# Performance work log

Measured on AMD Instinct MI355X. Metric: run time of the kernel, lower is better.

## Reference

```python
import jax, jax.numpy as jnp
import numpy as np

B, N, H, E, C = 32, 128, 8, 64, 16
D = H * E  # d_model


def auto_head_configs(n_heads, patch_num):
    candidates = set()
    for d in range(1, patch_num + 1):
        for K in (3, 5, 7):
            eff = (K - 1) * d + 1
            if eff <= patch_num and K <= patch_num and (K % 2 == 1):
                candidates.add((K, d, eff))
    gk = patch_num if patch_num % 2 == 1 else patch_num - 1
    gk = max(1, gk)
    candidates.add((gk, 1, gk))
    candidates = sorted(candidates, key=lambda x: (x[2], -x[0], x[1]))
    if not candidates:
        return [(1, 1)] * n_heads
    configs = []
    for h in range(n_heads):
        idx = round(h * (len(candidates) - 1) / max(1, n_heads - 1))
        idx = min(idx, len(candidates) - 1)
        configs.append((candidates[idx][0], candidates[idx][1]))
    return configs


def build_na_mask(n_heads, patch_num):
    mask = np.zeros((n_heads, patch_num, patch_num), dtype=bool)
    for h, (K, d) in enumerate(auto_head_configs(n_heads, patch_num)):
        pos = np.arange(patch_num)[:, None]                      # [N,1]
        ideal = pos + (np.arange(K) - K // 2) * d                # [N,K]
        valid = (ideal >= 0) & (ideal < patch_num)
        rows = np.broadcast_to(pos, ideal.shape)
        mask[h, rows[valid], ideal[valid]] = True
    return mask


def setup_inputs() -> dict:
    key = jax.random.key(0)
    kq, kk, kv, k1, k2 = jax.random.split(key, 5)
    return {
        "queries": jax.random.normal(kq, (B, N, H, E), dtype=jnp.float32),
        "keys": jax.random.normal(kk, (B, C, N, H, E), dtype=jnp.float32),
        "values": jax.random.normal(kv, (B, C, N, H, E), dtype=jnp.float32),
        "w1": jax.random.normal(k1, (D, D // 4), dtype=jnp.float32) * 0.02,
        "b1": jnp.zeros((D // 4,), dtype=jnp.float32),
        "w2": jax.random.normal(k2, (D // 4, 1), dtype=jnp.float32) * 0.02,
        "b2": jnp.zeros((1,), dtype=jnp.float32),
        "na_mask": jnp.asarray(build_na_mask(H, N)),  # [H,N,N] bool
    }


def reference(queries, keys, values, w1, b1, w2, b2, na_mask):
    Bb, Nn, Hh, Ee = queries.shape
    Cc = keys.shape[1]
    scale = Ee ** (-0.5)
    # per-exo-variable gate from mean-pooled values
    v_pool = values.mean(axis=2).reshape(Bb, Cc, Hh * Ee)           # [B,C,D]
    hid = jax.nn.gelu(v_pool @ w1 + b1, approximate=False)
    gate = jax.nn.sigmoid(hid @ w2 + b2)                             # [B,C,1]
    q = queries.transpose(0, 2, 1, 3)                                # [B,H,N,E]
    k_cat = keys.transpose(0, 3, 1, 2, 4).reshape(Bb, Hh, Cc * Nn, Ee)
    v_g = values * gate[:, :, :, None, None]                         # [B,C,N,H,E]
    v_cat = v_g.transpose(0, 3, 1, 2, 4).reshape(Bb, Hh, Cc * Nn, Ee)
    # mask [H,N,N] -> [H,N,C*N] (same neighborhood replicated per exo var)
    tmask = jnp.broadcast_to(na_mask[:, :, None, :], (Hh, Nn, Cc, Nn)).reshape(Hh, Nn, Cc * Nn)
    attn = jnp.einsum('bhne,bhme->bhnm', q, k_cat) * scale
    attn = jnp.where(tmask, attn, -jnp.inf)
    attn = jax.nn.softmax(attn, axis=-1)
    out = jnp.einsum('bhnm,bhme->bhne', attn, v_cat)
    return out.transpose(0, 2, 1, 3)                                 # [B,N,H,E]
```

## Files before the change

### kernel.cpp

```cpp
#include <hip/hip_runtime.h>
#include <hip/hip_bf16.h>
#include <math.h>

#define BB 32
#define NN 128
#define HH 8
#define EE 64
#define CC 16
#define DD 512

#define NEG_BIG (-1.0e30f)

__device__ __forceinline__ float bf2f(unsigned short u) {
    union { unsigned int i; float f; } x; x.i = ((unsigned int)u) << 16; return x.f;
}
__device__ __forceinline__ float bflo(unsigned int u) {
    union { unsigned int i; float f; } x; x.i = u << 16; return x.f;
}
__device__ __forceinline__ float bfhi(unsigned int u) {
    union { unsigned int i; float f; } x; x.i = u & 0xffff0000u; return x.f;
}
__device__ __forceinline__ unsigned short f2bf(float f) {
    union { float f; unsigned int i; } x; x.f = f;
    unsigned int r = x.i + 0x7fffu + ((x.i >> 16) & 1u);
    return (unsigned short)(r >> 16);
}

template <bool F32>
__device__ __forceinline__ float ldx(const void* p, int i) {
    if constexpr (F32) return ((const float*)p)[i];
    else               return bf2f(((const unsigned short*)p)[i]);
}

__device__ __forceinline__ void wave_lds_sync() {
    asm volatile("s_waitcnt lgkmcnt(0)" ::: "memory");
    __builtin_amdgcn_wave_barrier();
}

__device__ const int g_dil[8] = {1, 5, 19, 14, 37, 23, 55, 63};

__global__ void detect_dtype(const unsigned short* __restrict__ q, int* __restrict__ flag) {
    const int lane = threadIdx.x;
    int outliers = 0;
    #pragma unroll
    for (int i = 0; i < 16; ++i) {
        unsigned short u = q[(i * 64 + lane) * 2];
        int e = (u >> 7) & 0xFF;
        int sane = (e >= 101 && e <= 140) || ((u & 0x7FFFu) == 0);
        outliers += !sane;
    }
    #pragma unroll
    for (int m = 32; m >= 1; m >>= 1) outliers += __shfl_xor(outliers, m, 64);
    if (lane == 0) *flag = (outliers > 256) ? 1 : 0;
}

template <bool F32>
__global__ __launch_bounds__(1024) void gate_kernel(
    const void* __restrict__ values,
    const void* __restrict__ w1,
    const void* __restrict__ b1,
    const void* __restrict__ w2,
    const void* __restrict__ b2,
    const int*  __restrict__ flag,
    float* __restrict__ gate_out)
{
    if (*flag != (F32 ? 1 : 0)) return;
    __shared__ float vps[4][DD];
    __shared__ float vp[DD];
    __shared__ float hidp[4][DD / 4];
    __shared__ float hid[DD / 4];
    const int bc  = blockIdx.x;
    const int t   = threadIdx.x;
    const int grp = t >> 8;
    const int tt  = t & 255;
    float a0 = 0.f, a1 = 0.f;
    if constexpr (F32) {
        const float2* vb = (const float2*)((const float*)values + (size_t)bc * NN * DD)
                           + (size_t)(grp * 32) * (DD / 2);
        #pragma unroll 8
        for (int n = 0; n < 32; ++n) { float2 u = vb[n * (DD / 2) + tt]; a0 += u.x; a1 += u.y; }
    } else {
        const unsigned int* vb = (const unsigned int*)((const unsigned short*)values + (size_t)bc * NN * DD)
                                 + (size_t)(grp * 32) * (DD / 2);
        #pragma unroll 8
        for (int n = 0; n < 32; ++n) { unsigned int u = vb[n * (DD / 2) + tt]; a0 += bflo(u); a1 += bfhi(u); }
    }
    vps[grp][2 * tt]     = a0;
    vps[grp][2 * tt + 1] = a1;
    __syncthreads();
    if (t < 256) {
        float s0 = vps[0][2 * t]     + vps[1][2 * t]     + vps[2][2 * t]     + vps[3][2 * t];
        float s1 = vps[0][2 * t + 1] + vps[1][2 * t + 1] + vps[2][2 * t + 1] + vps[3][2 * t + 1];
        vp[2 * t]     = s0 * (1.0f / NN);
        vp[2 * t + 1] = s1 * (1.0f / NN);
    }
    __syncthreads();
    if (t < 512) {
        const int o  = t & 127;
        const int ch = t >> 7;
        float a = 0.f;
        #pragma unroll 4
        for (int dd = ch * 128; dd < ch * 128 + 128; ++dd)
            a += vp[dd] * ldx<F32>(w1, dd * (DD / 4) + o);
        hidp[ch][o] = a;
    }
    __syncthreads();
    if (t < 128) {
        float a = ldx<F32>(b1, t) + hidp[0][t] + hidp[1][t] + hidp[2][t] + hidp[3][t];
        hid[t] = 0.5f * a * (1.0f + erff(a * 0.70710678118654752440f));
    }
    __syncthreads();
    if (t < 64) {
        float s = hid[t] * ldx<F32>(w2, t) + hid[t + 64] * ldx<F32>(w2, t + 64);
        #pragma unroll
        for (int m = 32; m >= 1; m >>= 1) s += __shfl_xor(s, m, 64);
        if (t == 0) {
            float z = s + ldx<F32>(b2, 0);
            gate_out[bc] = 1.0f / (1.0f + expf(-z));
        }
    }
}

template <bool F32>
__global__ __launch_bounds__(256) void attn_kernel(
    const void* __restrict__ qptr,
    const void* __restrict__ kptr,
    const void* __restrict__ vptr,
    const float* __restrict__ gate,
    const int*  __restrict__ flag,
    void* __restrict__ optr)
{
    if (*flag != (F32 ? 1 : 0)) return;
    __shared__ float lds_w[4][CC * 5];
    const int tid  = threadIdx.x;
    const int wave = tid >> 6;
    const int lane = tid & 63;

    const int p    = blockIdx.x;
    const int virt = ((p & 7) << 10) | (p >> 3);
    const int gw   = virt * 4 + wave;
    const int n = gw & (NN - 1);
    const int h = (gw >> 7) & (HH - 1);
    const int b = gw >> 10;
    const int K   = ((h & 1) && (h != 7)) ? 5 : 3;
    const int dil = g_dil[h];
    const int nb  = CC * K;

    const int g   = lane >> 2;
    const int sub = lane & 3;

    const size_t qoff  = (((size_t)b * NN + n) * HH + h) * EE;
    const size_t kvoff = ((size_t)b * CC * NN) * DD + (size_t)h * EE;

    float qreg[16];
    if constexpr (F32) {
        const float4* qp = (const float4*)((const float*)qptr + qoff + sub * 16);
        #pragma unroll
        for (int i = 0; i < 4; ++i) {
            float4 u = qp[i];
            qreg[4 * i + 0] = u.x * 0.125f; qreg[4 * i + 1] = u.y * 0.125f;
            qreg[4 * i + 2] = u.z * 0.125f; qreg[4 * i + 3] = u.w * 0.125f;
        }
    } else {
        const uint4* qp = (const uint4*)((const unsigned short*)qptr + qoff + sub * 16);
        #pragma unroll
        for (int i = 0; i < 2; ++i) {
            uint4 u = qp[i];
            qreg[8 * i + 0] = bflo(u.x) * 0.125f; qreg[8 * i + 1] = bfhi(u.x) * 0.125f;
            qreg[8 * i + 2] = bflo(u.y) * 0.125f; qreg[8 * i + 3] = bfhi(u.y) * 0.125f;
            qreg[8 * i + 4] = bflo(u.z) * 0.125f; qreg[8 * i + 5] = bfhi(u.z) * 0.125f;
            qreg[8 * i + 6] = bflo(u.w) * 0.125f; qreg[8 * i + 7] = bfhi(u.w) * 0.125f;
        }
    }

    const size_t rowbase = kvoff + (size_t)g * NN * DD + (size_t)sub * 16;
    #pragma unroll 5
    for (int k = 0; k < K; ++k) {
        int jr = n + (k - (K >> 1)) * dil;
        bool valid = (jr >= 0) && (jr < NN);
        int j = valid ? jr : n;
        size_t off = rowbase + (size_t)j * DD;
        float a0 = 0.f, a1 = 0.f, a2 = 0.f, a3 = 0.f;
        if constexpr (F32) {
            const float4* kp = (const float4*)((const float*)kptr + off);
            #pragma unroll
            for (int i = 0; i < 4; ++i) {
                float4 kk = kp[i];
                a0 += qreg[4 * i + 0] * kk.x; a1 += qreg[4 * i + 1] * kk.y;
                a2 += qreg[4 * i + 2] * kk.z; a3 += qreg[4 * i + 3] * kk.w;
            }
        } else {
            const uint4* kp = (const uint4*)((const unsigned short*)kptr + off);
            #pragma unroll
            for (int i = 0; i < 2; ++i) {
                uint4 kk = kp[i];
                a0 += qreg[8 * i + 0] * bflo(kk.x); a1 += qreg[8 * i + 1] * bfhi(kk.x);
                a2 += qreg[8 * i + 2] * bflo(kk.y); a3 += qreg[8 * i + 3] * bfhi(kk.y);
                a0 += qreg[8 * i + 4] * bflo(kk.z); a1 += qreg[8 * i + 5] * bfhi(kk.z);
                a2 += qreg[8 * i + 6] * bflo(kk.w); a3 += qreg[8 * i + 7] * bfhi(kk.w);
            }
        }
        float s = (a0 + a1) + (a2 + a3);
        s += __shfl_xor(s, 1, 64);
        s += __shfl_xor(s, 2, 64);
        s = valid ? s : NEG_BIG;
        if (sub == 0) lds_w[wave][k * CC + g] = s;
    }
    wave_lds_sync();

    float s0 = (lane < nb) ? lds_w[wave][lane] : NEG_BIG;
    float s1 = (nb > 64 && lane + 64 < nb) ? lds_w[wave][lane + 64] : NEG_BIG;
    float m = fmaxf(s0, s1);
    #pragma unroll
    for (int mm = 32; mm >= 1; mm >>= 1) m = fmaxf(m, __shfl_xor(m, mm, 64));
    float e0 = (s0 <= NEG_BIG) ? 0.f : expf(s0 - m);
    float e1 = (s1 <= NEG_BIG) ? 0.f : expf(s1 - m);
    float tsum = e0 + e1;
    #pragma unroll
    for (int mm = 32; mm >= 1; mm >>= 1) tsum += __shfl_xor(tsum, mm, 64);
    float inv = 1.0f / tsum;
    float gv  = gate[b * CC + (lane & 15)];
    lds_w[wave][lane] = e0 * inv * gv;
    if (nb > 64 && lane + 64 < nb)
        lds_w[wave][lane + 64] = e1 * inv * gv;
    wave_lds_sync();

    const int e2   = lane & 31;
    const int cpar = lane >> 5;
    float acc0 = 0.f, acc1 = 0.f;
    #pragma unroll 5
    for (int k = 0; k < K; ++k) {
        int jr = n + (k - (K >> 1)) * dil;
        int j = (jr >= 0 && jr < NN) ? jr : n;
        const float* wrow = lds_w[wave] + k * CC;
        const size_t rbase = kvoff + (size_t)j * DD + 2 * e2;
        #pragma unroll
        for (int cc2 = 0; cc2 < CC / 2; ++cc2) {
            int c = 2 * cc2 + cpar;
            float w = wrow[c];
            size_t o = rbase + (size_t)c * (NN * DD);
            if constexpr (F32) {
                const float2 v = *(const float2*)((const float*)vptr + o);
                acc0 += w * v.x; acc1 += w * v.y;
            } else {
                unsigned int v = *(const unsigned int*)((const unsigned short*)vptr + o);
                acc0 += w * bflo(v); acc1 += w * bfhi(v);
            }
        }
    }
    acc0 += __shfl_xor(acc0, 32, 64);
    acc1 += __shfl_xor(acc1, 32, 64);
    if (lane < 32) {
        if constexpr (F32) {
            float2 r; r.x = acc0; r.y = acc1;
            ((float2*)((float*)optr + qoff))[e2] = r;
        } else {
            unsigned int pk = ((unsigned int)f2bf(acc1) << 16) | (unsigned int)f2bf(acc0);
            ((unsigned int*)((unsigned short*)optr + qoff))[e2] = pk;
        }
    }
}

extern "C" void kernel_launch(void* const* d_in, const int* in_sizes, int n_in,
                              void* d_out, int out_size, void* d_ws, size_t ws_size,
                              hipStream_t stream) {
    const void* queries = d_in[0];
    const void* keys    = d_in[1];
    const void* values  = d_in[2];
    const void* w1      = d_in[3];
    const void* b1      = d_in[4];
    const void* w2      = d_in[5];
    const void* b2      = d_in[6];

    int*   flag    = (int*)d_ws;
    float* gate_ws = (float*)d_ws + 64;

    hipLaunchKernelGGL(detect_dtype, dim3(1), dim3(64), 0, stream,
                       (const unsigned short*)queries, flag);
    hipLaunchKernelGGL((gate_kernel<false>), dim3(BB * CC), dim3(1024), 0, stream,
                       values, w1, b1, w2, b2, flag, gate_ws);
    hipLaunchKernelGGL((gate_kernel<true>), dim3(BB * CC), dim3(1024), 0, stream,
                       values, w1, b1, w2, b2, flag, gate_ws);
    hipLaunchKernelGGL((attn_kernel<false>), dim3(BB * HH * NN / 4), dim3(256), 0, stream,
                       queries, keys, values, gate_ws, flag, d_out);
    hipLaunchKernelGGL((attn_kernel<true>), dim3(BB * HH * NN / 4), dim3(256), 0, stream,
                       queries, keys, values, gate_ws, flag, d_out);
}
```

Measured before the change: 363.6 us.

## Merge dtype-templated launches, specialize attention on kernel size, skip invalid neighbors

Collapses the paired bf16/f32 kernel launches into single kernels that branch on the dtype flag, cutting two empty launches. The attention body is templated on K (3 or 5) so loops fully unroll, and out-of-range neighbors skip their K and V loads instead of reloading a clamped row. The V accumulation now has each lane own one output element and sum over all 16 channels directly, which removes the cross-half shuffle. Wave-local LDS syncs become block-wide __syncthreads; since all waves in a block share h, K is uniform across the block and the barrier is safe.

```diff
diff --git a/kernel.cpp b/kernel.cpp
--- a/kernel.cpp
+++ b/kernel.cpp
@@ -32,12 +32,7 @@
     else               return bf2f(((const unsigned short*)p)[i]);
 }
 
-__device__ __forceinline__ void wave_lds_sync() {
-    asm volatile("s_waitcnt lgkmcnt(0)" ::: "memory");
-    __builtin_amdgcn_wave_barrier();
-}
-
-__device__ const int g_dil[8] = {1, 5, 19, 14, 37, 23, 55, 63};
+#define DIL_PACK 0x3F3717250E130501ull
 
 __global__ void detect_dtype(const unsigned short* __restrict__ q, int* __restrict__ flag) {
     const int lane = threadIdx.x;
@@ -55,20 +50,12 @@
 }
 
 template <bool F32>
-__global__ __launch_bounds__(1024) void gate_kernel(
-    const void* __restrict__ values,
-    const void* __restrict__ w1,
-    const void* __restrict__ b1,
-    const void* __restrict__ w2,
-    const void* __restrict__ b2,
-    const int*  __restrict__ flag,
-    float* __restrict__ gate_out)
-{
-    if (*flag != (F32 ? 1 : 0)) return;
-    __shared__ float vps[4][DD];
-    __shared__ float vp[DD];
-    __shared__ float hidp[4][DD / 4];
-    __shared__ float hid[DD / 4];
+__device__ __forceinline__ void gate_body(
+    const void* __restrict__ values, const void* __restrict__ w1,
+    const void* __restrict__ b1, const void* __restrict__ w2,
+    const void* __restrict__ b2, float* __restrict__ gate_out,
+    float (&vps)[4][DD], float (&vp)[DD], float (&hidp)[4][DD / 4], float (&hid)[DD / 4])
+{
     const int bc  = blockIdx.x;
     const int t   = threadIdx.x;
     const int grp = t >> 8;
@@ -121,31 +108,29 @@
     }
 }
 
-template <bool F32>
-__global__ __launch_bounds__(256) void attn_kernel(
-    const void* __restrict__ qptr,
-    const void* __restrict__ kptr,
-    const void* __restrict__ vptr,
-    const float* __restrict__ gate,
-    const int*  __restrict__ flag,
-    void* __restrict__ optr)
-{
-    if (*flag != (F32 ? 1 : 0)) return;
-    __shared__ float lds_w[4][CC * 5];
-    const int tid  = threadIdx.x;
-    const int wave = tid >> 6;
-    const int lane = tid & 63;
-
-    const int p    = blockIdx.x;
-    const int virt = ((p & 7) << 10) | (p >> 3);
-    const int gw   = virt * 4 + wave;
-    const int n = gw & (NN - 1);
-    const int h = (gw >> 7) & (HH - 1);
-    const int b = gw >> 10;
-    const int K   = ((h & 1) && (h != 7)) ? 5 : 3;
-    const int dil = g_dil[h];
-    const int nb  = CC * K;
-
+__global__ __launch_bounds__(1024) void gate_kernel(
+    const void* __restrict__ values, const void* __restrict__ w1,
+    const void* __restrict__ b1, const void* __restrict__ w2,
+    const void* __restrict__ b2, const int* __restrict__ flag,
+    float* __restrict__ gate_out)
+{
+    __shared__ float vps[4][DD];
+    __shared__ float vp[DD];
+    __shared__ float hidp[4][DD / 4];
+    __shared__ float hid[DD / 4];
+    if (*flag) gate_body<true >(values, w1, b1, w2, b2, gate_out, vps, vp, hidp, hid);
+    else       gate_body<false>(values, w1, b1, w2, b2, gate_out, vps, vp, hidp, hid);
+}
+
+template <bool F32, int K>
+__device__ __forceinline__ void attn_body(
+    const void* __restrict__ qptr, const void* __restrict__ kptr,
+    const void* __restrict__ vptr, const float* __restrict__ gate,
+    void* __restrict__ optr,
+    int b, int h, int n, int dil, int wave, int lane,
+    float (&lds_w)[4][CC * 5])
+{
+    constexpr int nb = CC * K;
     const int g   = lane >> 2;
     const int sub = lane & 3;
 
@@ -174,42 +159,47 @@
     }
 
     const size_t rowbase = kvoff + (size_t)g * NN * DD + (size_t)sub * 16;
-    #pragma unroll 5
+    #pragma unroll
     for (int k = 0; k < K; ++k) {
-        int jr = n + (k - (K >> 1)) * dil;
-        bool valid = (jr >= 0) && (jr < NN);
-        int j = valid ? jr : n;
-        size_t off = rowbase + (size_t)j * DD;
-        float a0 = 0.f, a1 = 0.f, a2 = 0.f, a3 = 0.f;
-        if constexpr (F32) {
-            const float4* kp = (const float4*)((const float*)kptr + off);
-            #pragma unroll
-            for (int i = 0; i < 4; ++i) {
-                float4 kk = kp[i];
-                a0 += qreg[4 * i + 0] * kk.x; a1 += qreg[4 * i + 1] * kk.y;
-                a2 += qreg[4 * i + 2] * kk.z; a3 += qreg[4 * i + 3] * kk.w;
+        int j = n + (k - (K >> 1)) * dil;
+        float s = NEG_BIG;
+        if (j >= 0 && j < NN) {
+            size_t off = rowbase + (size_t)j * DD;
+            float a0 = 0.f, a1 = 0.f, a2 = 0.f, a3 = 0.f;
+            if constexpr (F32) {
+                const float4* kp = (const float4*)((const float*)kptr + off);
+                float4 kb[4];
+                #pragma unroll
+                for (int i = 0; i < 4; ++i) kb[i] = kp[i];
+                #pragma unroll
+                for (int i = 0; i < 4; ++i) {
+                    a0 += qreg[4 * i + 0] * kb[i].x; a1 += qreg[4 * i + 1] * kb[i].y;
+                    a2 += qreg[4 * i + 2] * kb[i].z; a3 += qreg[4 * i + 3] * kb[i].w;
+                }
+            } else {
+                const uint4* kp = (const uint4*)((const unsigned short*)kptr + off);
+                uint4 kb[2];
+                #pragma unroll
+                for (int i = 0; i < 2; ++i) kb[i] = kp[i];
+                #pragma unroll
+                for (int i = 0; i < 2; ++i) {
+                    a0 += qreg[8 * i + 0] * bflo(kb[i].x); a1 += qreg[8 * i + 1] * bfhi(kb[i].x);
+                    a2 += qreg[8 * i + 2] * bflo(kb[i].y); a3 += qreg[8 * i + 3] * bfhi(kb[i].y);
+                    a0 += qreg[8 * i + 4] * bflo(kb[i].z); a1 += qreg[8 * i + 5] * bfhi(kb[i].z);
+                    a2 += qreg[8 * i + 6] * bflo(kb[i].w); a3 += qreg[8 * i + 7] * bfhi(kb[i].w);
+                }
             }
-        } else {
-            const uint4* kp = (const uint4*)((const unsigned short*)kptr + off);
-            #pragma unroll
-            for (int i = 0; i < 2; ++i) {
-                uint4 kk = kp[i];
-                a0 += qreg[8 * i + 0] * bflo(kk.x); a1 += qreg[8 * i + 1] * bfhi(kk.x);
-                a2 += qreg[8 * i + 2] * bflo(kk.y); a3 += qreg[8 * i + 3] * bfhi(kk.y);
-                a0 += qreg[8 * i + 4] * bflo(kk.z); a1 += qreg[8 * i + 5] * bfhi(kk.z);
-                a2 += qreg[8 * i + 6] * bflo(kk.w); a3 += qreg[8 * i + 7] * bfhi(kk.w);
-            }
-        }
-        float s = (a0 + a1) + (a2 + a3);
-        s += __shfl_xor(s, 1, 64);
-        s += __shfl_xor(s, 2, 64);
-        s = valid ? s : NEG_BIG;
+            s = (a0 + a1) + (a2 + a3);
+            s += __shfl_xor(s, 1, 64);
+            s += __shfl_xor(s, 2, 64);
+        }
         if (sub == 0) lds_w[wave][k * CC + g] = s;
     }
-    wave_lds_sync();
+    __syncthreads();
 
     float s0 = (lane < nb) ? lds_w[wave][lane] : NEG_BIG;
-    float s1 = (nb > 64 && lane + 64 < nb) ? lds_w[wave][lane + 64] : NEG_BIG;
+    float s1 = NEG_BIG;
+    if constexpr (K == 5) { if (lane < nb - 64) s1 = lds_w[wave][lane + 64]; }
     float m = fmaxf(s0, s1);
     #pragma unroll
     for (int mm = 32; mm >= 1; mm >>= 1) m = fmaxf(m, __shfl_xor(m, mm, 64));
@@ -221,43 +211,59 @@
     float inv = 1.0f / tsum;
     float gv  = gate[b * CC + (lane & 15)];
     lds_w[wave][lane] = e0 * inv * gv;
-    if (nb > 64 && lane + 64 < nb)
-        lds_w[wave][lane + 64] = e1 * inv * gv;
-    wave_lds_sync();
-
-    const int e2   = lane & 31;
-    const int cpar = lane >> 5;
-    float acc0 = 0.f, acc1 = 0.f;
-    #pragma unroll 5
+    if constexpr (K == 5) { if (lane < nb - 64) lds_w[wave][lane + 64] = e1 * inv * gv; }
+    __syncthreads();
+
+    float acc = 0.f;
+    #pragma unroll
     for (int k = 0; k < K; ++k) {
-        int jr = n + (k - (K >> 1)) * dil;
-        int j = (jr >= 0 && jr < NN) ? jr : n;
+        int j = n + (k - (K >> 1)) * dil;
+        if (j < 0 || j >= NN) continue;
         const float* wrow = lds_w[wave] + k * CC;
-        const size_t rbase = kvoff + (size_t)j * DD + 2 * e2;
-        #pragma unroll
-        for (int cc2 = 0; cc2 < CC / 2; ++cc2) {
-            int c = 2 * cc2 + cpar;
-            float w = wrow[c];
-            size_t o = rbase + (size_t)c * (NN * DD);
-            if constexpr (F32) {
-                const float2 v = *(const float2*)((const float*)vptr + o);
-                acc0 += w * v.x; acc1 += w * v.y;
-            } else {
-                unsigned int v = *(const unsigned int*)((const unsigned short*)vptr + o);
-                acc0 += w * bflo(v); acc1 += w * bfhi(v);
-            }
-        }
-    }
-    acc0 += __shfl_xor(acc0, 32, 64);
-    acc1 += __shfl_xor(acc1, 32, 64);
-    if (lane < 32) {
+        const size_t base = kvoff + (size_t)j * DD + lane;
+        float vv[CC];
         if constexpr (F32) {
-            float2 r; r.x = acc0; r.y = acc1;
-            ((float2*)((float*)optr + qoff))[e2] = r;
+            const float* vb = (const float*)vptr + base;
+            #pragma unroll
+            for (int c = 0; c < CC; ++c) vv[c] = vb[(size_t)c * (NN * DD)];
         } else {
-            unsigned int pk = ((unsigned int)f2bf(acc1) << 16) | (unsigned int)f2bf(acc0);
-            ((unsigned int*)((unsigned short*)optr + qoff))[e2] = pk;
-        }
+            const unsigned short* vb = (const unsigned short*)vptr + base;
+            #pragma unroll
+            for (int c = 0; c < CC; ++c) vv[c] = bf2f(vb[(size_t)c * (NN * DD)]);
+        }
+        #pragma unroll
+        for (int c = 0; c < CC; ++c) acc += wrow[c] * vv[c];
+    }
+    if constexpr (F32) ((float*)optr)[qoff + lane] = acc;
+    else               ((unsigned short*)optr)[qoff + lane] = f2bf(acc);
+}
+
+__global__ __launch_bounds__(256) void attn_kernel(
+    const void* __restrict__ qptr, const void* __restrict__ kptr,
+    const void* __restrict__ vptr, const float* __restrict__ gate,
+    const int* __restrict__ flag, void* __restrict__ optr)
+{
+    __shared__ float lds_w[4][CC * 5];
+    const int tid  = threadIdx.x;
+    const int wave = tid >> 6;
+    const int lane = tid & 63;
+
+    const int p    = blockIdx.x;
+    const int virt = ((p & 7) << 10) | (p >> 3);
+    const int gw0  = virt * 4;
+    const int n    = (gw0 & (NN - 1)) + wave;
+    const int h    = (gw0 >> 7) & (HH - 1);
+    const int b    = gw0 >> 10;
+    const int dil  = (int)((DIL_PACK >> (h * 8)) & 0xFF);
+    const bool k5  = (h & 1) && (h != 7);
+
+    const int f = *flag;
+    if (f) {
+        if (k5) attn_body<true, 5>(qptr, kptr, vptr, gate, optr, b, h, n, dil, wave, lane, lds_w);
+        else    attn_body<true, 3>(qptr, kptr, vptr, gate, optr, b, h, n, dil, wave, lane, lds_w);
+    } else {
+        if (k5) attn_body<false, 5>(qptr, kptr, vptr, gate, optr, b, h, n, dil, wave, lane, lds_w);
+        else    attn_body<false, 3>(qptr, kptr, vptr, gate, optr, b, h, n, dil, wave, lane, lds_w);
     }
 }
 
@@ -277,12 +283,8 @@
 
     hipLaunchKernelGGL(detect_dtype, dim3(1), dim3(64), 0, stream,
                        (const unsigned short*)queries, flag);
-    hipLaunchKernelGGL((gate_kernel<false>), dim3(BB * CC), dim3(1024), 0, stream,
+    hipLaunchKernelGGL(gate_kernel, dim3(BB * CC), dim3(1024), 0, stream,
                        values, w1, b1, w2, b2, flag, gate_ws);
-    hipLaunchKernelGGL((gate_kernel<true>), dim3(BB * CC), dim3(1024), 0, stream,
-                       values, w1, b1, w2, b2, flag, gate_ws);
-    hipLaunchKernelGGL((attn_kernel<false>), dim3(BB * HH * NN / 4), dim3(256), 0, stream,
+    hipLaunchKernelGGL(attn_kernel, dim3(BB * HH * NN / 4), dim3(256), 0, stream,
                        queries, keys, values, gate_ws, flag, d_out);
-    hipLaunchKernelGGL((attn_kernel<true>), dim3(BB * HH * NN / 4), dim3(256), 0, stream,
-                       queries, keys, values, gate_ws, flag, d_out);
-}
+}
```

Result: faster. 339.0 us (-6.7%).
